# Performance work log

Hardware: AMD Instinct MI355X
Metric: run time of the kernel (lower is better)

## Reference

```python
import jax, jax.numpy as jnp
import numpy as np

# ---- config (from cfg / InstantNGP defaults) ----
W_IMG, H_IMG = 1024, 1024            # uv_reso_w, uv_reso_h
N_LEVELS = 16                        # standard InstantNGP level count
BASE_RES = 16
FINEST_RES = 1024                    # cfg['finest_level']
F_FEAT = 2                           # features per level
LOG2_T = 19                          # cfg['log2_hashmap_size']
T = 1 << LOG2_T
HIDDEN = 64
PRIMES = np.array([1, 2654435761], dtype=np.uint32)  # 2D spatial-hash primes


def setup_inputs() -> dict:
    key = jax.random.key(0)
    ks = jax.random.split(key, 5)
    d_in = N_LEVELS * F_FEAT
    tables = jax.random.uniform(ks[0], (N_LEVELS, T, F_FEAT), jnp.float32, -1e-4, 1e-4)
    W1 = jax.random.normal(ks[1], (d_in, HIDDEN), jnp.float32) / np.sqrt(d_in)
    b1 = jnp.zeros((HIDDEN,), jnp.float32)
    W2 = jax.random.normal(ks[2], (HIDDEN, HIDDEN), jnp.float32) / np.sqrt(HIDDEN)
    b2 = jnp.zeros((HIDDEN,), jnp.float32)
    W3 = jax.random.normal(ks[3], (HIDDEN, 3), jnp.float32) / np.sqrt(HIDDEN)
    b3 = jnp.zeros((3,), jnp.float32)
    return {"tables": tables, "W1": W1, "b1": b1, "W2": W2, "b2": b2, "W3": W3, "b3": b3}


def _uv_coords():
    # replicate torch.meshgrid(arange(W), arange(H), indexing='xy') -> (H, W)
    xx, yy = jnp.meshgrid(jnp.arange(W_IMG), jnp.arange(H_IMG), indexing='xy')
    x = xx.ravel().astype(jnp.float32) / W_IMG
    y = yy.ravel().astype(jnp.float32) / H_IMG
    return jnp.stack([x, y], axis=1)  # [N, 2]


def _hash_encode(coord, tables):
    # coord: [N,2] in [0,1); tables: [L,T,F]
    growth = np.exp((np.log(FINEST_RES) - np.log(BASE_RES)) / (N_LEVELS - 1))
    res = np.floor(BASE_RES * growth ** np.arange(N_LEVELS)).astype(np.float32)  # [L]
    scaled = coord[None, :, :] * res[:, None, None]          # [L,N,2]
    c0f = jnp.floor(scaled)
    frac = scaled - c0f                                       # [L,N,2]
    c0 = c0f.astype(jnp.uint32)
    corners = jnp.array([[0, 0], [1, 0], [0, 1], [1, 1]], dtype=jnp.uint32)  # [4,2]
    cc = c0[:, :, None, :] + corners[None, None]              # [L,N,4,2]
    idx = (cc[..., 0] * jnp.uint32(PRIMES[0])) ^ (cc[..., 1] * jnp.uint32(PRIMES[1]))
    idx = (idx & jnp.uint32(T - 1)).astype(jnp.int32)         # [L,N,4]
    feats = jax.vmap(lambda tab, i: tab[i])(tables, idx)      # [L,N,4,F] scattered gather
    cf = corners.astype(jnp.float32)                          # [4,2]
    # bilinear weights: prod over dims of (frac if corner bit else 1-frac)
    w = jnp.prod(cf[None, None] * frac[:, :, None, :] +
                 (1.0 - cf[None, None]) * (1.0 - frac[:, :, None, :]), axis=-1)  # [L,N,4]
    feat = jnp.einsum('lnc,lncf->lnf', w, feats)              # [L,N,F]
    return jnp.transpose(feat, (1, 0, 2)).reshape(-1, N_LEVELS * F_FEAT)  # [N, L*F]


def reference(tables, W1, b1, W2, b2, W3, b3):
    coord = _uv_coords()                                      # [N,2]
    enc = _hash_encode(coord, tables)                         # [N,32]
    h = jax.nn.relu(enc @ W1 + b1)
    h = jax.nn.relu(h @ W2 + b2)
    out = h @ W3 + b3                                         # [N,3]
    img = out.reshape(H_IMG, W_IMG, 3).transpose(2, 0, 1)     # [3,H,W]
    return jax.nn.sigmoid(img)[None, ...]                     # [1,3,H,W]
```

## Files before the change

### kernel.cpp

```cpp
#include <hip/hip_runtime.h>
#include <math.h>

#define NLEV   16
#define TSIZE  524288
#define TMASK  524287
#define NPIX   (1024*1024)
#define NCORN  908
#define MAP_F_OFF 3600

typedef __attribute__((ext_vector_type(8))) short s8v;
typedef __attribute__((ext_vector_type(4))) float f4v;
typedef __attribute__((ext_vector_type(2))) float f2v;

struct ResArr { float r[NLEV]; };
union Frag { unsigned int u[4]; s8v v; };

#define WC0 3
#define WC_LIST  {3,3,3,3,3,3,4,4,5,5,6,7,9,11,14,17}
#define OFF_LIST {0,9,18,27,36,45,54,70,86,111,136,172,221,302,423,619}

__device__ __forceinline__ unsigned short bf16_rn(float x) {
    unsigned int u = __builtin_bit_cast(unsigned int, x);
    u += 0x7fffu + ((u >> 16) & 1u);
    return (unsigned short)(u >> 16);
}
__device__ __forceinline__ unsigned int pk_bf16(float lo, float hi) {
    return __builtin_amdgcn_perm(__builtin_bit_cast(unsigned int, hi),
                                 __builtin_bit_cast(unsigned int, lo),
                                 0x07060302u);
}

__global__ __launch_bounds__(256) void prep_kernel(
    const float* __restrict__ W1, const float* __restrict__ W2,
    const float* __restrict__ W3, float* __restrict__ ws, ResArr res)
{
    const int t = threadIdx.x;
    if (t < NLEV) ws[t] = res.r[t];
    unsigned short* w1t = (unsigned short*)(ws + 16);
    unsigned short* w2t = w1t + 64 * 32;
    unsigned short* w3t = w2t + 64 * 64;
    unsigned int*   map = (unsigned int*)(ws + MAP_F_OFF);
    for (int i = t; i < 64 * 32; i += 256) {
        int n = i >> 5, k = i & 31;
        w1t[i] = bf16_rn(W1[k * 64 + n]);
    }
    for (int i = t; i < 64 * 64; i += 256) {
        int n2 = i >> 6, kp = i & 63;
        int klog = (kp & 32) | ((kp & 4) << 2) | ((kp & 24) >> 1) | (kp & 3);
        w2t[i] = bf16_rn(W2[klog * 64 + n2]);
    }
    for (int i = t; i < 16 * 64; i += 256) {
        int row = i >> 6, kp = i & 63;
        int klog = (kp & 32) | ((kp & 4) << 2) | ((kp & 24) >> 1) | (kp & 3);
        int ch = row & 3;
        w3t[i] = (ch < 3) ? bf16_rn(W3[klog * 3 + ch]) : (unsigned short)0;
    }
    constexpr int WCc[16]  = WC_LIST;
    constexpr int OFFc[16] = OFF_LIST;
    for (int i = t; i < NCORN; i += 256) {
        int l = 0, off = 0, wc = WC0;
        #pragma unroll
        for (int k = 1; k < 16; ++k)
            if (i >= OFFc[k]) { l = k; off = OFFc[k]; wc = WCc[k]; }
        const int loc = i - off;
        const int jj  = loc / wc;
        const int ii  = loc - jj * wc;
        map[i] = ((unsigned int)l << 16) | ((unsigned int)jj << 8)
               | (unsigned int)ii;
    }
}

__global__ __launch_bounds__(256) void ngp_fused_kernel(
    const float* __restrict__ tables,
    const float* __restrict__ b1, const float* __restrict__ b2,
    const float* __restrict__ b3,
    const float* __restrict__ ws, float* __restrict__ out)
{
    __shared__ float2 ldsc[NCORN];

    const int tid  = threadIdx.x;
    const int lane = tid & 63;
    const int wv   = tid >> 6;
    const int c15  = lane & 15;
    const int g    = lane >> 4;
    const int xb   = blockIdx.x * 16;
    const int yb   = blockIdx.y * 16;

    const float xbf = (float)xb * (1.0f / 1024.0f);
    const float ybf = (float)yb * (1.0f / 1024.0f);

    {
        const unsigned int* __restrict__ map =
            (const unsigned int*)(ws + MAP_F_OFF);
        const float2* __restrict__ tabs = (const float2*)tables;
        for (int i = tid; i < NCORN; i += 256) {
            const unsigned int m = map[i];
            const int l  = (int)(m >> 16);
            const int jj = (int)((m >> 8) & 255u);
            const int ii = (int)(m & 255u);
            const float r = ws[l];
            const int cx0 = (int)floorf(xbf * r);
            const int cy0 = (int)floorf(ybf * r);
            const unsigned int idx =
                (((unsigned int)(cx0 + ii)) ^
                 ((unsigned int)(cy0 + jj) * 2654435761u)) & TMASK;
            ldsc[i] = tabs[((size_t)l << 19) + idx];
        }
    }
    __syncthreads();

    const float4 rv = *(const float4*)(ws + g * 4);
    const float rr[4] = { rv.x, rv.y, rv.z, rv.w };
    const float xs = (float)(xb + c15) * (1.0f / 1024.0f);
    float yf[4];
    #pragma unroll
    for (int pt = 0; pt < 4; ++pt)
        yf[pt] = (float)(yb + wv * 4 + pt) * (1.0f / 1024.0f);

    constexpr int WCc[16]  = WC_LIST;
    constexpr int OFFc[16] = OFF_LIST;
    Frag bfrag[4];
    #pragma unroll
    for (int j = 0; j < 4; ++j) {
        int wc  = WCc[j];      int off = OFFc[j];
        wc  = (g == 1) ? WCc[4 + j]  : wc;  off = (g == 1) ? OFFc[4 + j]  : off;
        wc  = (g == 2) ? WCc[8 + j]  : wc;  off = (g == 2) ? OFFc[8 + j]  : off;
        wc  = (g == 3) ? WCc[12 + j] : wc;  off = (g == 3) ? OFFc[12 + j] : off;
        const float r   = rr[j];
        const float sx  = xs * r;
        const float fx0 = floorf(sx);
        const float fx  = sx - fx0;
        const f2v  fx2  = { fx, fx };
        const int ii    = (int)fx0 - (int)floorf(xbf * r);
        const int cy0i  = (int)floorf(ybf * r);
        const int rowb  = off + ii;
        #pragma unroll
        for (int pt = 0; pt < 4; ++pt) {
            const float sy  = yf[pt] * r;
            const float fy0 = floorf(sy);
            const float fy  = sy - fy0;
            const f2v  fy2  = { fy, fy };
            const int jj    = (int)fy0 - cy0i;
            const int base  = rowb + jj * wc;
            const f2v c00 = *(const f2v*)&ldsc[base];
            const f2v c10 = *(const f2v*)&ldsc[base + 1];
            const f2v c01 = *(const f2v*)&ldsc[base + wc];
            const f2v c11 = *(const f2v*)&ldsc[base + wc + 1];
            const f2v top = c00 + fx2 * (c10 - c00);
            const f2v bot = c01 + fx2 * (c11 - c01);
            const f2v e   = top + fy2 * (bot - top);
            bfrag[pt].u[j] = pk_bf16(e[0], e[1]);
        }
    }

    const unsigned short* __restrict__ w1t = (const unsigned short*)(ws + 16);
    const unsigned short* __restrict__ w2t = w1t + 64 * 32;
    const unsigned short* __restrict__ w3t = w2t + 64 * 64;
    const f4v zero4 = { 0.f, 0.f, 0.f, 0.f };

    Frag hp2[2][4];
    #pragma unroll
    for (int mt = 0; mt < 4; ++mt) {
        Frag afr;
        afr.v = *(const s8v*)(w1t + (mt * 16 + c15) * 32 + g * 8);
        const f4v bb = *(const f4v*)(b1 + mt * 16 + g * 4);
        #pragma unroll
        for (int pt = 0; pt < 4; ++pt) {
            f4v acc = zero4;
            acc = __builtin_amdgcn_mfma_f32_16x16x32_bf16(
                afr.v, bfrag[pt].v, acc, 0, 0, 0);
            const f4v hv = __builtin_elementwise_max(acc + bb, zero4);
            hp2[mt >> 1][pt].u[(mt & 1) * 2 + 0] = pk_bf16(hv[0], hv[1]);
            hp2[mt >> 1][pt].u[(mt & 1) * 2 + 1] = pk_bf16(hv[2], hv[3]);
        }
    }

    Frag hq2[2][4];
    #pragma unroll
    for (int mt = 0; mt < 4; ++mt) {
        const f4v bb2 = *(const f4v*)(b2 + mt * 16 + g * 4);
        f4v acc[4] = { zero4, zero4, zero4, zero4 };
        #pragma unroll
        for (int st = 0; st < 2; ++st) {
            Frag a2;
            a2.v = *(const s8v*)(w2t + (mt * 16 + c15) * 64 + st * 32 + g * 8);
            #pragma unroll
            for (int pt = 0; pt < 4; ++pt)
                acc[pt] = __builtin_amdgcn_mfma_f32_16x16x32_bf16(
                    a2.v, hp2[st][pt].v, acc[pt], 0, 0, 0);
        }
        #pragma unroll
        for (int pt = 0; pt < 4; ++pt) {
            const f4v hv = __builtin_elementwise_max(acc[pt] + bb2, zero4);
            hq2[mt >> 1][pt].u[(mt & 1) * 2 + 0] = pk_bf16(hv[0], hv[1]);
            hq2[mt >> 1][pt].u[(mt & 1) * 2 + 1] = pk_bf16(hv[2], hv[3]);
        }
    }

    f4v acc3[4] = { zero4, zero4, zero4, zero4 };
    #pragma unroll
    for (int st = 0; st < 2; ++st) {
        Frag a3;
        a3.v = *(const s8v*)(w3t + c15 * 64 + st * 32 + g * 8);
        #pragma unroll
        for (int pt = 0; pt < 4; ++pt)
            acc3[pt] = __builtin_amdgcn_mfma_f32_16x16x32_bf16(
                a3.v, hq2[st][pt].v, acc3[pt], 0, 0, 0);
    }

    float ov[3];
    #pragma unroll
    for (int c = 0; c < 3; ++c) {
        float v = acc3[0][c];
        v = (g == 1) ? acc3[1][c] : v;
        v = (g == 2) ? acc3[2][c] : v;
        v = (g == 3) ? acc3[3][c] : v;
        ov[c] = v + b3[c];
    }
    const int pix = ((yb + wv * 4 + g) << 10) + xb + c15;
    out[0 * NPIX + pix] = 1.0f / (1.0f + __expf(-ov[0]));
    out[1 * NPIX + pix] = 1.0f / (1.0f + __expf(-ov[1]));
    out[2 * NPIX + pix] = 1.0f / (1.0f + __expf(-ov[2]));
}

extern "C" void kernel_launch(void* const* d_in, const int* in_sizes, int n_in,
                              void* d_out, int out_size, void* d_ws, size_t ws_size,
                              hipStream_t stream) {
    const float* tables = (const float*)d_in[0];
    const float* W1     = (const float*)d_in[1];
    const float* b1     = (const float*)d_in[2];
    const float* W2     = (const float*)d_in[3];
    const float* b2     = (const float*)d_in[4];
    const float* W3     = (const float*)d_in[5];
    const float* b3     = (const float*)d_in[6];
    float* out          = (float*)d_out;
    float* ws           = (float*)d_ws;

    ResArr res;
    const double growth = exp((log(1024.0) - log(16.0)) / 15.0);
    for (int l = 0; l < NLEV; ++l)
        res.r[l] = (float)floor(16.0 * pow(growth, (double)l));

    hipLaunchKernelGGL(prep_kernel, dim3(1), dim3(256), 0, stream, W1, W2, W3, ws, res);
    hipLaunchKernelGGL(ngp_fused_kernel, dim3(64, 64), dim3(256), 0, stream,
                       tables, b1, b2, b3, ws, out);
}
```

Baseline: 70.11 us.

## Give each wavefront its own hash-corner LDS tile and drop block barrier

Instead of the whole 256-thread block cooperatively gathering a 16x16-pixel corner set into shared LDS and then synchronizing, each wavefront now gathers the corners for its own 16x4 strip into a private LDS region. This removes the __syncthreads barrier and lets wavefronts proceed independently, overlapping gather latency with other wavefronts' MLP work. The trade-off is more total gather traffic, since the per-wave corner sets overlap, plus padding slots and a larger LDS footprint. Reads within a wave rely on implicit wave-level ordering of LDS stores and loads.

```diff
diff --git a/kernel.cpp b/kernel.cpp
--- a/kernel.cpp
+++ b/kernel.cpp
@@ -5,7 +5,7 @@
 #define TSIZE  524288
 #define TMASK  524287
 #define NPIX   (1024*1024)
-#define NCORN  908
+#define NWC    448
 #define MAP_F_OFF 3600
 
 typedef __attribute__((ext_vector_type(8))) short s8v;
@@ -15,9 +15,9 @@
 struct ResArr { float r[NLEV]; };
 union Frag { unsigned int u[4]; s8v v; };
 
-#define WC0 3
-#define WC_LIST  {3,3,3,3,3,3,4,4,5,5,6,7,9,11,14,17}
-#define OFF_LIST {0,9,18,27,36,45,54,70,86,111,136,172,221,302,423,619}
+#define WCX_LIST {3,3,3,3,3,3,4,4,5,5,6,7,9,11,14,18}
+#define WCY_LIST {3,3,3,3,3,3,3,3,3,3,3,3,4,4,5,6}
+#define OFF_LIST {0,9,18,27,36,45,54,66,78,93,108,126,147,183,227,297}
 
 __device__ __forceinline__ unsigned short bf16_rn(float x) {
     unsigned int u = __builtin_bit_cast(unsigned int, x);
@@ -55,18 +55,22 @@
         int ch = row & 3;
         w3t[i] = (ch < 3) ? bf16_rn(W3[klog * 3 + ch]) : (unsigned short)0;
     }
-    constexpr int WCc[16]  = WC_LIST;
+    constexpr int WCXc[16] = WCX_LIST;
     constexpr int OFFc[16] = OFF_LIST;
-    for (int i = t; i < NCORN; i += 256) {
-        int l = 0, off = 0, wc = WC0;
-        #pragma unroll
-        for (int k = 1; k < 16; ++k)
-            if (i >= OFFc[k]) { l = k; off = OFFc[k]; wc = WCc[k]; }
-        const int loc = i - off;
-        const int jj  = loc / wc;
-        const int ii  = loc - jj * wc;
-        map[i] = ((unsigned int)l << 16) | ((unsigned int)jj << 8)
-               | (unsigned int)ii;
+    for (int i = t; i < NWC; i += 256) {
+        unsigned int m = 0;
+        if (i < 405) {
+            int l = 0, off = 0, wc = 3;
+            #pragma unroll
+            for (int k = 1; k < 16; ++k)
+                if (i >= OFFc[k]) { l = k; off = OFFc[k]; wc = WCXc[k]; }
+            const int loc = i - off;
+            const int jj  = loc / wc;
+            const int ii  = loc - jj * wc;
+            m = ((unsigned int)l << 16) | ((unsigned int)jj << 8)
+              | (unsigned int)ii;
+        }
+        map[i] = m;
     }
 }
 
@@ -76,7 +80,7 @@
     const float* __restrict__ b3,
     const float* __restrict__ ws, float* __restrict__ out)
 {
-    __shared__ float2 ldsc[NCORN];
+    __shared__ float2 ldsw[4][NWC];
 
     const int tid  = threadIdx.x;
     const int lane = tid & 63;
@@ -85,29 +89,32 @@
     const int g    = lane >> 4;
     const int xb   = blockIdx.x * 16;
     const int yb   = blockIdx.y * 16;
+    const int yw   = yb + wv * 4;
 
     const float xbf = (float)xb * (1.0f / 1024.0f);
-    const float ybf = (float)yb * (1.0f / 1024.0f);
+    const float ywf = (float)yw * (1.0f / 1024.0f);
 
     {
         const unsigned int* __restrict__ map =
             (const unsigned int*)(ws + MAP_F_OFF);
         const float2* __restrict__ tabs = (const float2*)tables;
-        for (int i = tid; i < NCORN; i += 256) {
-            const unsigned int m = map[i];
+        float2* __restrict__ dst = &ldsw[wv][0];
+        #pragma unroll
+        for (int it = 0; it < 7; ++it) {
+            const int s = it * 64 + lane;
+            const unsigned int m = map[s];
             const int l  = (int)(m >> 16);
             const int jj = (int)((m >> 8) & 255u);
             const int ii = (int)(m & 255u);
             const float r = ws[l];
             const int cx0 = (int)floorf(xbf * r);
-            const int cy0 = (int)floorf(ybf * r);
+            const int cy0 = (int)floorf(ywf * r);
             const unsigned int idx =
                 (((unsigned int)(cx0 + ii)) ^
                  ((unsigned int)(cy0 + jj) * 2654435761u)) & TMASK;
-            ldsc[i] = tabs[((size_t)l << 19) + idx];
-        }
-    }
-    __syncthreads();
+            dst[s] = tabs[((size_t)l << 19) + idx];
+        }
+    }
 
     const float4 rv = *(const float4*)(ws + g * 4);
     const float rr[4] = { rv.x, rv.y, rv.z, rv.w };
@@ -115,24 +122,25 @@
     float yf[4];
     #pragma unroll
     for (int pt = 0; pt < 4; ++pt)
-        yf[pt] = (float)(yb + wv * 4 + pt) * (1.0f / 1024.0f);
-
-    constexpr int WCc[16]  = WC_LIST;
+        yf[pt] = (float)(yw + pt) * (1.0f / 1024.0f);
+
+    constexpr int WCXc[16] = WCX_LIST;
     constexpr int OFFc[16] = OFF_LIST;
+    const float2* __restrict__ lw = &ldsw[wv][0];
     Frag bfrag[4];
     #pragma unroll
     for (int j = 0; j < 4; ++j) {
-        int wc  = WCc[j];      int off = OFFc[j];
-        wc  = (g == 1) ? WCc[4 + j]  : wc;  off = (g == 1) ? OFFc[4 + j]  : off;
-        wc  = (g == 2) ? WCc[8 + j]  : wc;  off = (g == 2) ? OFFc[8 + j]  : off;
-        wc  = (g == 3) ? WCc[12 + j] : wc;  off = (g == 3) ? OFFc[12 + j] : off;
+        int wc  = WCXc[j];     int off = OFFc[j];
+        wc  = (g == 1) ? WCXc[4 + j]  : wc;  off = (g == 1) ? OFFc[4 + j]  : off;
+        wc  = (g == 2) ? WCXc[8 + j]  : wc;  off = (g == 2) ? OFFc[8 + j]  : off;
+        wc  = (g == 3) ? WCXc[12 + j] : wc;  off = (g == 3) ? OFFc[12 + j] : off;
         const float r   = rr[j];
         const float sx  = xs * r;
         const float fx0 = floorf(sx);
         const float fx  = sx - fx0;
         const f2v  fx2  = { fx, fx };
         const int ii    = (int)fx0 - (int)floorf(xbf * r);
-        const int cy0i  = (int)floorf(ybf * r);
+        const int cy0i  = (int)floorf(ywf * r);
         const int rowb  = off + ii;
         #pragma unroll
         for (int pt = 0; pt < 4; ++pt) {
@@ -142,10 +150,10 @@
             const f2v  fy2  = { fy, fy };
             const int jj    = (int)fy0 - cy0i;
             const int base  = rowb + jj * wc;
-            const f2v c00 = *(const f2v*)&ldsc[base];
-            const f2v c10 = *(const f2v*)&ldsc[base + 1];
-            const f2v c01 = *(const f2v*)&ldsc[base + wc];
-            const f2v c11 = *(const f2v*)&ldsc[base + wc + 1];
+            const f2v c00 = *(const f2v*)&lw[base];
+            const f2v c10 = *(const f2v*)&lw[base + 1];
+            const f2v c01 = *(const f2v*)&lw[base + wc];
+            const f2v c11 = *(const f2v*)&lw[base + wc + 1];
             const f2v top = c00 + fx2 * (c10 - c00);
             const f2v bot = c01 + fx2 * (c11 - c01);
             const f2v e   = top + fy2 * (bot - top);
@@ -217,7 +225,7 @@
         v = (g == 3) ? acc3[3][c] : v;
         ov[c] = v + b3[c];
     }
-    const int pix = ((yb + wv * 4 + g) << 10) + xb + c15;
+    const int pix = ((yw + g) << 10) + xb + c15;
     out[0 * NPIX + pix] = 1.0f / (1.0f + __expf(-ov[0]));
     out[1 * NPIX + pix] = 1.0f / (1.0f + __expf(-ov[1]));
     out[2 * NPIX + pix] = 1.0f / (1.0f + __expf(-ov[2]));
```

Result: no change. 69.77 us (-0.5%).
